# Performance work log

Hardware: AMD Instinct MI355X
Metric: run time of the kernel (lower is better)

Reference implementation:

```python
import jax, jax.numpy as jnp
import numpy as np

N_ATOMS = 50000
N_EDGES = 1600000
DIM = 128
N_FILTERS = 128
OUT_DIM = 128
N_GAUSS = 50
CUTOFF = 10.0
LOG2 = float(np.log(2.0))


def ssp(x):
    # ShiftedSoftplus: softplus(x) - log(2)
    return jax.nn.softplus(x) - LOG2


def setup_inputs() -> dict:
    key = jax.random.key(0)
    ks = jax.random.split(key, 10)
    inp = {}
    inp["x"] = jax.random.normal(ks[0], (N_ATOMS, DIM), dtype=jnp.float32)
    inp["r_ij"] = jax.random.uniform(ks[1], (N_EDGES,), dtype=jnp.float32) * CUTOFF
    inp["f_ij"] = jax.random.normal(ks[2], (N_EDGES, N_GAUSS), dtype=jnp.float32)
    inp["ind_i"] = jax.random.randint(ks[3], (N_EDGES,), 0, N_ATOMS)
    inp["ind_j"] = jax.random.randint(ks[4], (N_EDGES,), 0, N_ATOMS)
    # filter network: Linear(50,128) + SSP + Linear(128,128) + SSP
    inp["Wf1"] = jax.random.normal(ks[5], (N_GAUSS, N_FILTERS), dtype=jnp.float32) / np.sqrt(N_GAUSS)
    inp["bf1"] = jnp.zeros((N_FILTERS,), dtype=jnp.float32)
    inp["Wf2"] = jax.random.normal(ks[6], (N_FILTERS, N_FILTERS), dtype=jnp.float32) / np.sqrt(N_FILTERS)
    inp["bf2"] = jnp.zeros((N_FILTERS,), dtype=jnp.float32)
    # in2f: Linear(dim, n_filters, bias=False)
    inp["Win"] = jax.random.normal(ks[7], (DIM, N_FILTERS), dtype=jnp.float32) / np.sqrt(DIM)
    # f2out: Linear(n_filters, out_dim) + SSP
    inp["Wout"] = jax.random.normal(ks[8], (N_FILTERS, OUT_DIM), dtype=jnp.float32) / np.sqrt(N_FILTERS)
    inp["bout"] = jnp.zeros((OUT_DIM,), dtype=jnp.float32)
    return inp


def reference(x, r_ij, f_ij, ind_i, ind_j, Wf1, bf1, Wf2, bf2, Win, Wout, bout):
    # filter network on edge features: [E, n_gauss] -> [E, n_filters]
    W = ssp(f_ij @ Wf1 + bf1)
    W = ssp(W @ Wf2 + bf2)
    # cosine cutoff: [E]
    C = 0.5 * (jnp.cos(r_ij * (jnp.pi / CUTOFF)) + 1.0)
    C = C * (r_ij < CUTOFF).astype(C.dtype)
    W = W * C[:, None]
    # node projection: [N, dim] -> [N, n_filters]
    h = x @ Win
    # gather neighbor features, apply filter, scatter-add by ind_i
    m = h[ind_j] * W                                   # [E, n_filters]
    agg = jax.ops.segment_sum(m, ind_i, num_segments=x.shape[0])  # [N, n_filters]
    # f2out: Linear + ShiftedSoftplus
    return ssp(agg @ Wout + bout)
```

## Files before the change

kernel.cpp:

```cpp
#include <hip/hip_runtime.h>
#include <math.h>

#define N_ATOMS 50000
#define N_EDGES 1600000
#define NF 128
#define NG 50
#define ITERS 4
#define EPB 512
#define LOG2F_ 0.69314718055994530942f
#define PI_OVER_CUT 0.31415926535897932f
#define CUTOFF_F 10.0f

typedef _Float16 half_t;
typedef _Float16 f16x8 __attribute__((ext_vector_type(8)));
typedef _Float16 f16x2 __attribute__((ext_vector_type(2)));
typedef float f32x4 __attribute__((ext_vector_type(4)));
typedef unsigned int u32x4 __attribute__((ext_vector_type(4)));

__device__ __forceinline__ float sspf_fast(float x) {
    float e = __expf(-fabsf(x));
    float l = __logf(1.0f + e);
    return fmaxf(x, 0.0f) + (l - LOG2F_);
}

__device__ __forceinline__ unsigned short f2h_bits(float x) {
    half_t h = (half_t)x;
    return __builtin_bit_cast(unsigned short, h);
}

__device__ __forceinline__ unsigned int pk2(float a, float b) {
    return __builtin_bit_cast(unsigned int, __builtin_amdgcn_cvt_pkrtz(a, b));
}

template <bool BIAS_SSP, bool IN_HALF, bool OUT_HALF>
__global__ __launch_bounds__(256) void gemm128_kernel(
    const void* __restrict__ Xv, const float* __restrict__ W,
    const float* __restrict__ bias, void* __restrict__ Yv, int N) {
    __shared__ float xs[32][128];
    const int row0 = blockIdx.x * 32;
    const int tid = threadIdx.x;

    if (IN_HALF) {
        const half_t* X = (const half_t*)Xv;
        for (int i = tid; i < 32 * 16; i += 256) {
            int r = i >> 4;
            f16x8 v = {0, 0, 0, 0, 0, 0, 0, 0};
            if (row0 + r < N) v = *((const f16x8*)(X + (size_t)row0 * 128) + i);
            #pragma unroll
            for (int e = 0; e < 8; ++e) xs[r][(i & 15) * 8 + e] = (float)v[e];
        }
    } else {
        const float4* src = (const float4*)((const float*)Xv + (size_t)row0 * 128);
        float4* dst = (float4*)(&xs[0][0]);
        for (int i = tid; i < 32 * 32; i += 256) {
            int r = i >> 5;
            float4 v = {0.f, 0.f, 0.f, 0.f};
            if (row0 + r < N) v = src[i];
            dst[i] = v;
        }
    }
    __syncthreads();

    const int rq = tid >> 5;
    const int cq = tid & 31;
    float4 a0 = {0,0,0,0}, a1 = {0,0,0,0}, a2 = {0,0,0,0}, a3 = {0,0,0,0};
    const float4* Wv = (const float4*)W;

    #pragma unroll 4
    for (int k = 0; k < 128; ++k) {
        float4 w = Wv[k * 32 + cq];
        float x0 = xs[rq * 4 + 0][k];
        float x1 = xs[rq * 4 + 1][k];
        float x2 = xs[rq * 4 + 2][k];
        float x3 = xs[rq * 4 + 3][k];
        a0.x += x0 * w.x; a0.y += x0 * w.y; a0.z += x0 * w.z; a0.w += x0 * w.w;
        a1.x += x1 * w.x; a1.y += x1 * w.y; a1.z += x1 * w.z; a1.w += x1 * w.w;
        a2.x += x2 * w.x; a2.y += x2 * w.y; a2.z += x2 * w.z; a2.w += x2 * w.w;
        a3.x += x3 * w.x; a3.y += x3 * w.y; a3.z += x3 * w.z; a3.w += x3 * w.w;
    }

    float4 bq = {0,0,0,0};
    if (BIAS_SSP) bq = ((const float4*)bias)[cq];
    #pragma unroll
    for (int i = 0; i < 4; ++i) {
        float4 v = (i == 0) ? a0 : (i == 1) ? a1 : (i == 2) ? a2 : a3;
        int r = row0 + rq * 4 + i;
        if (r >= N) continue;
        if (BIAS_SSP) {
            v.x = sspf_fast(v.x + bq.x); v.y = sspf_fast(v.y + bq.y);
            v.z = sspf_fast(v.z + bq.z); v.w = sspf_fast(v.w + bq.w);
        }
        if (OUT_HALF) {
            uint2 st = { pk2(v.x, v.y), pk2(v.z, v.w) };
            *(uint2*)((half_t*)Yv + (size_t)r * 128 + cq * 4) = st;
        } else {
            ((float4*)((float*)Yv + (size_t)r * 128))[cq] = v;
        }
    }
}

__global__ __launch_bounds__(256) void preconv_kernel(
    const float* __restrict__ Wf1, const float* __restrict__ Wf2,
    half_t* __restrict__ w1t, half_t* __restrict__ w2t) {
    int id = blockIdx.x * 256 + threadIdx.x;
    if (id < 128 * 64) {
        int col = id >> 6, k = id & 63;
        w1t[id] = (k < NG) ? (half_t)Wf1[k * NF + col] : (half_t)0.0f;
    } else if (id < 128 * 64 + 128 * 128) {
        int t = id - 128 * 64;
        int col = t >> 7, k = t & 127;
        w2t[t] = (half_t)Wf2[k * NF + col];
    }
}

#define OFF_W2T   16384
#define OFF_W1OUT 49152

__global__ __launch_bounds__(512, 4) void edge_kernel(
    const float* __restrict__ f_ij, const float* __restrict__ r_ij,
    const int* __restrict__ ind_i, const int* __restrict__ ind_j,
    const half_t* __restrict__ w1t_g, const half_t* __restrict__ w2t_g,
    const float* __restrict__ bf1, const float* __restrict__ bf2,
    const half_t* __restrict__ h, float* __restrict__ agg) {
    __shared__ __align__(16) unsigned char lds[81920];
    const int tid = threadIdx.x;

    for (int c = tid; c < 1024; c += 512) {
        int col = c >> 3, kc = c & 7;
        u32x4 v = ((const u32x4*)w1t_g)[c];
        *(u32x4*)(lds + (col << 7) + ((kc ^ (col & 7)) << 4)) = v;
    }
    for (int c = tid; c < 2048; c += 512) {
        int col = c >> 4, kc = c & 15;
        u32x4 v = ((const u32x4*)w2t_g)[c];
        int slot = (kc & 8) | ((kc & 7) ^ (col & 7));
        *(u32x4*)(lds + OFF_W2T + (col << 8) + (slot << 4)) = v;
    }

    const int lane = tid & 63;
    const int wid = tid >> 6;
    const int l15 = lane & 15;
    const int lg  = lane >> 4;
    const int l7  = lane & 7;
    const int h3  = l15 >> 3;
    const int hb  = (l7 >> 2) & 1;
    const int lgl = lg ^ (l7 & 3);

    float b1r[8], b2r[8];
    #pragma unroll
    for (int t = 0; t < 8; ++t) {
        b1r[t] = bf1[t * 16 + l15];
        b2r[t] = bf2[t * 16 + l15];
    }

    const int b1b0 = (l15 << 7) + (hb << 6) + (lgl << 4);
    const int b1b1 = (l15 << 7) + ((hb ^ 1) << 6) + (lgl << 4);
    const int b2b0 = OFF_W2T + (l15 << 8) + (hb << 6) + (lgl << 4);
    const int b2b1 = OFF_W2T + (l15 << 8) + ((hb ^ 1) << 6) + (lgl << 4);
    const int a2b0 = OFF_W1OUT + wid * 4096 + (l15 << 8) + (hb << 6) + (lgl << 4);
    const int a2b1 = OFF_W1OUT + wid * 4096 + (l15 << 8) + ((hb ^ 1) << 6) + (lgl << 4);
    const int ep1base = OFF_W1OUT + wid * 4096 + lg * 1024 + l7 * 2;
    const int rw4 = (lg & 1) * 4;

    const int bb = blockIdx.x * EPB;
    const float* aptr = f_ij + (size_t)(bb + wid * 16 + l15) * NG + lg * 8;

    __syncthreads();

    for (int it = 0; it < ITERS; ++it) {
        const int eb = bb + it * 128 + wid * 16;
        const int erow = eb + lg * 4;

        float rv[4]; int jv[4], iv[4];
        #pragma unroll
        for (int r = 0; r < 4; ++r) {
            rv[r] = r_ij[erow + r];
            jv[r] = ind_j[erow + r];
            iv[r] = ind_i[erow + r];
        }

        float2 q[8];
        #pragma unroll
        for (int p = 0; p < 4; ++p) q[p] = *(const float2*)(aptr + 2 * p);
        #pragma unroll
        for (int p = 0; p < 4; ++p) {
            float2 v = {0.f, 0.f};
            if (lg * 8 + 2 * p <= 16) v = *(const float2*)(aptr + 32 + 2 * p);
            q[4 + p] = v;
        }
        aptr += (size_t)128 * NG;

        unsigned short hs[4][8];
        #pragma unroll
        for (int r = 0; r < 4; ++r) {
            const unsigned short* hrow =
                (const unsigned short*)(h + (size_t)jv[r] * NF) + l15;
            #pragma unroll
            for (int t = 0; t < 8; ++t) hs[r][t] = hrow[t * 16];
        }

        f16x8 a1[2];
        #pragma unroll
        for (int ks = 0; ks < 2; ++ks) {
            #pragma unroll
            for (int p = 0; p < 4; ++p) {
                f16x2 hvv = __builtin_bit_cast(f16x2,
                    __builtin_amdgcn_cvt_pkrtz(q[ks * 4 + p].x, q[ks * 4 + p].y));
                a1[ks][2 * p]     = hvv[0];
                a1[ks][2 * p + 1] = hvv[1];
            }
        }

        f32x4 acc1[8];
        #pragma unroll
        for (int t = 0; t < 8; ++t) acc1[t] = (f32x4){0.f, 0.f, 0.f, 0.f};
        __builtin_amdgcn_s_setprio(1);
        #pragma unroll
        for (int t = 0; t < 8; ++t) {
            f16x8 b0 = *(const f16x8*)(lds + b1b0 + t * 2048);
            f16x8 b1 = *(const f16x8*)(lds + b1b1 + t * 2048);
            acc1[t] = __builtin_amdgcn_mfma_f32_16x16x32_f16(a1[0], b0, acc1[t], 0, 0, 0);
            acc1[t] = __builtin_amdgcn_mfma_f32_16x16x32_f16(a1[1], b1, acc1[t], 0, 0, 0);
        }
        __builtin_amdgcn_s_setprio(0);

        #pragma unroll
        for (int t = 0; t < 8; ++t) {
            #pragma unroll
            for (int r = 0; r < 4; ++r) {
                unsigned short bits = f2h_bits(sspf_fast(acc1[t][r] + b1r[t]));
                int slotx = (2 * (t & 3) + h3) ^ (rw4 + r);
                *(unsigned short*)(lds + ep1base + r * 256 + ((t >> 2) << 7) + (slotx << 4)) = bits;
            }
        }

        f32x4 acc2[8];
        #pragma unroll
        for (int t = 0; t < 8; ++t) acc2[t] = (f32x4){0.f, 0.f, 0.f, 0.f};
        f16x8 a2[4];
        #pragma unroll
        for (int ks = 0; ks < 4; ++ks) {
            int addr = ((ks & 1) ? a2b1 : a2b0) + (ks >> 1) * 128;
            a2[ks] = *(const f16x8*)(lds + addr);
        }
        __builtin_amdgcn_s_setprio(1);
        #pragma unroll
        for (int t = 0; t < 8; ++t) {
            #pragma unroll
            for (int ks = 0; ks < 4; ++ks) {
                int addr = ((ks & 1) ? b2b1 : b2b0) + (ks >> 1) * 128 + t * 4096;
                f16x8 b = *(const f16x8*)(lds + addr);
                acc2[t] = __builtin_amdgcn_mfma_f32_16x16x32_f16(a2[ks], b, acc2[t], 0, 0, 0);
            }
        }
        __builtin_amdgcn_s_setprio(0);

        #pragma unroll
        for (int r = 0; r < 4; ++r) {
            float c = 0.5f * (__cosf(rv[r] * PI_OVER_CUT) + 1.0f);
            c = (rv[r] < CUTOFF_F) ? c : 0.0f;
            float* grow = agg + (size_t)iv[r] * NF + l15;
            #pragma unroll
            for (int t = 0; t < 8; ++t) {
                float w2 = sspf_fast(acc2[t][r] + b2r[t]) * c;
                float hf = (float)__builtin_bit_cast(half_t, hs[r][t]);
                atomicAdd(grow + t * 16, hf * w2);
            }
        }
    }
}

extern "C" void kernel_launch(void* const* d_in, const int* in_sizes, int n_in,
                              void* d_out, int out_size, void* d_ws, size_t ws_size,
                              hipStream_t stream) {
    const float* x     = (const float*)d_in[0];
    const float* r_ij  = (const float*)d_in[1];
    const float* f_ij  = (const float*)d_in[2];
    const int*   ind_i = (const int*)d_in[3];
    const int*   ind_j = (const int*)d_in[4];
    const float* Wf1   = (const float*)d_in[5];
    const float* bf1   = (const float*)d_in[6];
    const float* Wf2   = (const float*)d_in[7];
    const float* bf2   = (const float*)d_in[8];
    const float* Win   = (const float*)d_in[9];
    const float* Wout  = (const float*)d_in[10];
    const float* bout  = (const float*)d_in[11];
    float* out = (float*)d_out;

    float*  agg = (float*)d_ws;
    half_t* h   = (half_t*)(agg + (size_t)N_ATOMS * NF);
    half_t* w1t = h + (size_t)N_ATOMS * NF;
    half_t* w2t = w1t + 128 * 64;

    (void)hipMemsetAsync(agg, 0, (size_t)N_ATOMS * NF * sizeof(float), stream);

    preconv_kernel<<<96, 256, 0, stream>>>(Wf1, Wf2, w1t, w2t);

    const int gemm_blocks = (N_ATOMS + 31) / 32;
    gemm128_kernel<false, false, true><<<gemm_blocks, 256, 0, stream>>>(
        x, Win, nullptr, h, N_ATOMS);

    edge_kernel<<<N_EDGES / EPB, 512, 0, stream>>>(f_ij, r_ij, ind_i, ind_j,
                                                   w1t, w2t, bf1, bf2, h, agg);

    gemm128_kernel<true, false, false><<<gemm_blocks, 256, 0, stream>>>(
        agg, Wout, bout, out, N_ATOMS);
}
```

Measured before the change: 758.3 us.

## Read filter weights directly from global memory instead of staging in LDS

Drops the per-block copy of the transposed fp16 filter weights into shared memory and the barrier after it. MFMA B fragments are now loaded straight from global memory, relying on L1/L2 caching. This shrinks LDS use from 80 KB to 32 KB per block so more blocks can fit on a CU, and removes the setprio hints. The cost is more vector-memory traffic per iteration, and weight-load latency now sits in front of the MFMAs.

```diff
diff --git a/kernel.cpp b/kernel.cpp
--- a/kernel.cpp
+++ b/kernel.cpp
@@ -113,29 +113,14 @@
     }
 }
 
-#define OFF_W2T   16384
-#define OFF_W1OUT 49152
-
 __global__ __launch_bounds__(512, 4) void edge_kernel(
     const float* __restrict__ f_ij, const float* __restrict__ r_ij,
     const int* __restrict__ ind_i, const int* __restrict__ ind_j,
     const half_t* __restrict__ w1t_g, const half_t* __restrict__ w2t_g,
     const float* __restrict__ bf1, const float* __restrict__ bf2,
     const half_t* __restrict__ h, float* __restrict__ agg) {
-    __shared__ __align__(16) unsigned char lds[81920];
+    __shared__ __align__(16) unsigned char lds[32768];
     const int tid = threadIdx.x;
-
-    for (int c = tid; c < 1024; c += 512) {
-        int col = c >> 3, kc = c & 7;
-        u32x4 v = ((const u32x4*)w1t_g)[c];
-        *(u32x4*)(lds + (col << 7) + ((kc ^ (col & 7)) << 4)) = v;
-    }
-    for (int c = tid; c < 2048; c += 512) {
-        int col = c >> 4, kc = c & 15;
-        u32x4 v = ((const u32x4*)w2t_g)[c];
-        int slot = (kc & 8) | ((kc & 7) ^ (col & 7));
-        *(u32x4*)(lds + OFF_W2T + (col << 8) + (slot << 4)) = v;
-    }
 
     const int lane = tid & 63;
     const int wid = tid >> 6;
@@ -153,19 +138,16 @@
         b2r[t] = bf2[t * 16 + l15];
     }
 
-    const int b1b0 = (l15 << 7) + (hb << 6) + (lgl << 4);
-    const int b1b1 = (l15 << 7) + ((hb ^ 1) << 6) + (lgl << 4);
-    const int b2b0 = OFF_W2T + (l15 << 8) + (hb << 6) + (lgl << 4);
-    const int b2b1 = OFF_W2T + (l15 << 8) + ((hb ^ 1) << 6) + (lgl << 4);
-    const int a2b0 = OFF_W1OUT + wid * 4096 + (l15 << 8) + (hb << 6) + (lgl << 4);
-    const int a2b1 = OFF_W1OUT + wid * 4096 + (l15 << 8) + ((hb ^ 1) << 6) + (lgl << 4);
-    const int ep1base = OFF_W1OUT + wid * 4096 + lg * 1024 + l7 * 2;
+    const half_t* w1p = w1t_g + l15 * 64 + lg * 8;
+    const half_t* w2p = w2t_g + l15 * 128 + lg * 8;
+
+    const int a2b0 = wid * 4096 + (l15 << 8) + (hb << 6) + (lgl << 4);
+    const int a2b1 = wid * 4096 + (l15 << 8) + ((hb ^ 1) << 6) + (lgl << 4);
+    const int ep1base = wid * 4096 + lg * 1024 + l7 * 2;
     const int rw4 = (lg & 1) * 4;
 
     const int bb = blockIdx.x * EPB;
     const float* aptr = f_ij + (size_t)(bb + wid * 16 + l15) * NG + lg * 8;
-
-    __syncthreads();
 
     for (int it = 0; it < ITERS; ++it) {
         const int eb = bb + it * 128 + wid * 16;
@@ -214,15 +196,13 @@
         f32x4 acc1[8];
         #pragma unroll
         for (int t = 0; t < 8; ++t) acc1[t] = (f32x4){0.f, 0.f, 0.f, 0.f};
-        __builtin_amdgcn_s_setprio(1);
         #pragma unroll
         for (int t = 0; t < 8; ++t) {
-            f16x8 b0 = *(const f16x8*)(lds + b1b0 + t * 2048);
-            f16x8 b1 = *(const f16x8*)(lds + b1b1 + t * 2048);
+            f16x8 b0 = *(const f16x8*)(w1p + t * 1024);
+            f16x8 b1 = *(const f16x8*)(w1p + t * 1024 + 32);
             acc1[t] = __builtin_amdgcn_mfma_f32_16x16x32_f16(a1[0], b0, acc1[t], 0, 0, 0);
             acc1[t] = __builtin_amdgcn_mfma_f32_16x16x32_f16(a1[1], b1, acc1[t], 0, 0, 0);
         }
-        __builtin_amdgcn_s_setprio(0);
 
         #pragma unroll
         for (int t = 0; t < 8; ++t) {
@@ -243,17 +223,14 @@
             int addr = ((ks & 1) ? a2b1 : a2b0) + (ks >> 1) * 128;
             a2[ks] = *(const f16x8*)(lds + addr);
         }
-        __builtin_amdgcn_s_setprio(1);
         #pragma unroll
         for (int t = 0; t < 8; ++t) {
             #pragma unroll
             for (int ks = 0; ks < 4; ++ks) {
-                int addr = ((ks & 1) ? b2b1 : b2b0) + (ks >> 1) * 128 + t * 4096;
-                f16x8 b = *(const f16x8*)(lds + addr);
+                f16x8 b = *(const f16x8*)(w2p + t * 2048 + ks * 32);
                 acc2[t] = __builtin_amdgcn_mfma_f32_16x16x32_f16(a2[ks], b, acc2[t], 0, 0, 0);
             }
         }
-        __builtin_amdgcn_s_setprio(0);
 
         #pragma unroll
         for (int r = 0; r < 4; ++r) {
```

New measurement: 1.464 ms. +93.1%, slower.
